# Performance work log

Measured on AMD Instinct MI355X. Metric: run time of the kernel, lower is better.

The kernel has to match this reference:

```python
import jax, jax.numpy as jnp
import numpy as np

SEQ_LEN = 4096
EMBED_DIM = 1280
NUM_HEADS = 16
HEAD_DIM = EMBED_DIM // NUM_HEADS  # 80
SCALING = float(np.sqrt(HEAD_DIM))  # NOTE: source multiplies by sqrt(head_dim)
NEG_INF = float(np.finfo(np.float32).min)


def rotate_half(x):
    x1, x2 = jnp.split(x, 2, axis=-1)
    return jnp.concatenate((-x2, x1), axis=-1)


def setup_inputs() -> dict:
    key = jax.random.key(0)
    ks = jax.random.split(key, 7)
    s = 0.02
    hidden_states = jax.random.normal(ks[0], (SEQ_LEN, EMBED_DIM), dtype=jnp.float32)
    w_qkv = jax.random.normal(ks[1], (3 * EMBED_DIM, EMBED_DIM), dtype=jnp.float32) * s
    b_qkv = jax.random.normal(ks[2], (3 * EMBED_DIM,), dtype=jnp.float32) * s
    w_proj = jax.random.normal(ks[3], (EMBED_DIM, EMBED_DIM), dtype=jnp.float32) * s
    b_proj = jax.random.normal(ks[4], (EMBED_DIM,), dtype=jnp.float32) * s
    # rotary angles: theta duplicated to head_dim (emb = cat(rope, rope))
    inv_freq = 1.0 / (10000.0 ** (jnp.arange(0, HEAD_DIM // 2, dtype=jnp.float32) * 2.0 / HEAD_DIM))
    pos = jnp.arange(SEQ_LEN, dtype=jnp.float32)
    freqs = pos[:, None] * inv_freq[None, :]            # [S, hd/2]
    emb = jnp.concatenate((freqs, freqs), axis=-1)       # [S, hd]
    cos = jnp.cos(emb)
    sin = jnp.sin(emb)
    # 4 packed images of 1024 patches each
    cu_seqlens = jnp.array([0, 1024, 2048, 3072, 4096], dtype=jnp.int32)
    return {
        "hidden_states": hidden_states,
        "w_qkv": w_qkv, "b_qkv": b_qkv,
        "w_proj": w_proj, "b_proj": b_proj,
        "cos": cos, "sin": sin,
        "cu_seqlens": cu_seqlens,
    }


def reference(hidden_states, w_qkv, b_qkv, w_proj, b_proj, cos, sin, cu_seqlens):
    S = hidden_states.shape[0]
    # packed QKV projection
    qkv = hidden_states @ w_qkv.T + b_qkv                  # [S, 3D]
    qkv = qkv.reshape(S, 3, NUM_HEADS, HEAD_DIM)
    q, k, v = qkv[:, 0], qkv[:, 1], qkv[:, 2]              # [S, H, hd]
    # fp32 RoPE (broadcast cos/sin over heads)
    c = cos[:, None, :].astype(jnp.float32)
    sn = sin[:, None, :].astype(jnp.float32)
    qf, kf = q.astype(jnp.float32), k.astype(jnp.float32)
    q = (qf * c + rotate_half(qf) * sn).astype(q.dtype)
    k = (kf * c + rotate_half(kf) * sn).astype(k.dtype)
    # block-diagonal mask from cu_seqlens: same segment -> 0, else -inf
    pos = jnp.arange(S)
    seg = jnp.searchsorted(cu_seqlens, pos, side="right") - 1  # [S]
    bias = jnp.where(seg[:, None] == seg[None, :], 0.0, NEG_INF)  # [S, S]
    # dense attention over whole packed sequence (as in source)
    scores = jnp.einsum("shd,thd->hst", q, k) * SCALING + bias[None]
    weights = jax.nn.softmax(scores.astype(jnp.float32), axis=-1).astype(q.dtype)
    attn = jnp.einsum("hst,thd->shd", weights, v).reshape(S, EMBED_DIM)
    return attn @ w_proj.T + b_proj
```

## Files before the change

kernel.cpp:

```cpp
#include <hip/hip_runtime.h>

#define SEQ   4096
#define EMB   1280
#define NH    16
#define HD    80
#define HDP   96
#define O3    3840
#define SEGLEN 1024
#define NSEG  4
#define QSCALE (8.94427190999915878564f * 1.44269504088896340736f)

typedef unsigned short u16;
typedef __attribute__((ext_vector_type(8))) _Float16 f16x8;
typedef __attribute__((ext_vector_type(4))) _Float16 f16x4;
typedef __attribute__((ext_vector_type(2))) __fp16   h16x2;
typedef __attribute__((ext_vector_type(4))) float    f32x4;

__device__ __forceinline__ float ex2(float x) { return __builtin_amdgcn_exp2f(x); }

__device__ __forceinline__ u16 f2h(float f) {
  union { _Float16 h; u16 u; } v; v.h = (_Float16)f; return v.u;
}
__device__ __forceinline__ float h2f(u16 b) {
  union { u16 u; _Float16 h; } v; v.u = b; return (float)v.h;
}
__device__ __forceinline__ f32x4 exp2_4(f32x4 x) {
  f32x4 r; r.x = ex2(x.x); r.y = ex2(x.y); r.z = ex2(x.z); r.w = ex2(x.w); return r;
}
__device__ __forceinline__ f16x4 pk4(f32x4 s) {
  union { h16x2 h[2]; f16x4 f; } u;
  u.h[0] = __builtin_amdgcn_cvt_pkrtz(s.x, s.y);
  u.h[1] = __builtin_amdgcn_cvt_pkrtz(s.z, s.w);
  return u.f;
}
__device__ __forceinline__ void gl2lds16(const u16* g, u16* l) {
  __builtin_amdgcn_global_load_lds(
      (const __attribute__((address_space(1))) unsigned int*)g,
      (__attribute__((address_space(3))) unsigned int*)l, 16, 0, 0);
}

#define CVT_N1 (SEQ * EMB / 4)
#define CVT_N2 (O3 * EMB / 4)
#define CVT_N3 (EMB * EMB / 4)
__global__ void cvt_all_kernel(const float* __restrict__ a, const float* __restrict__ b,
                               const float* __restrict__ c, u16* __restrict__ oa,
                               u16* __restrict__ ob, u16* __restrict__ oc) {
  int i = blockIdx.x * blockDim.x + threadIdx.x;
  const float* src; u16* dst; int j = i;
  if (j < CVT_N1)                { src = a; dst = oa; }
  else if (j < CVT_N1 + CVT_N2)  { src = b; dst = ob; j -= CVT_N1; }
  else                           { src = c; dst = oc; j -= CVT_N1 + CVT_N2; }
  float4 f = ((const float4*)src)[j];
  union { u16 h[4]; uint2 v; } o;
  o.h[0] = f2h(f.x); o.h[1] = f2h(f.y); o.h[2] = f2h(f.z); o.h[3] = f2h(f.w);
  ((uint2*)dst)[j] = o.v;
}

template<int OUTF>
__global__ __launch_bounds__(256)
void gemm_bias_kernel(const u16* __restrict__ A, const u16* __restrict__ W,
                      const float* __restrict__ bias, void* __restrict__ Cout,
                      int N, int K) {
  __shared__ u16 As[128][64];
  __shared__ u16 Bs[128][64];
  const int tid  = threadIdx.x;
  const int flat = blockIdx.x + gridDim.x * blockIdx.y;
  const int cpx  = (gridDim.x * gridDim.y) >> 3;
  const int nid  = (flat & 7) * cpx + (flat >> 3);
  const int bm   = nid / gridDim.x, bn = nid % gridDim.x;
  const int lane = tid & 63;
  const int wid  = tid >> 6;
  const int wm   = (wid >> 1) * 64, wn = (wid & 1) * 64;
  const int lr   = lane & 15, quad = lane >> 4;

  f32x4 acc[4][4];
  const f32x4 z4 = {0.f, 0.f, 0.f, 0.f};
  #pragma unroll
  for (int i = 0; i < 4; ++i)
    #pragma unroll
    for (int j = 0; j < 4; ++j) acc[i][j] = z4;

  const int arow = tid >> 3;
  const int acol = (((tid & 7) ^ (arow & 7)) * 8);
  const u16* Ab = A + (size_t)(bm * 128) * K;
  const u16* Wb = W + (size_t)(bn * 128) * K;
  u16* AsL = &As[0][0] + tid * 8;
  u16* BsL = &Bs[0][0] + tid * 8;

  for (int kt = 0; kt < K; kt += 64) {
    #pragma unroll
    for (int r = 0; r < 4; ++r) {
      gl2lds16(&Ab[(size_t)(arow + r * 32) * K + kt + acol], AsL + r * 2048);
      gl2lds16(&Wb[(size_t)(arow + r * 32) * K + kt + acol], BsL + r * 2048);
    }
    __syncthreads();
    #pragma unroll
    for (int k32 = 0; k32 < 2; ++k32) {
      const int c = (((k32 * 4 + quad) ^ (lr & 7)) * 8);
      f16x8 aF[4], bF[4];
      #pragma unroll
      for (int i = 0; i < 4; ++i) {
        aF[i] = *(const f16x8*)&As[wm + i * 16 + lr][c];
        bF[i] = *(const f16x8*)&Bs[wn + i * 16 + lr][c];
      }
      #pragma unroll
      for (int i = 0; i < 4; ++i)
        #pragma unroll
        for (int j = 0; j < 4; ++j)
          acc[i][j] = __builtin_amdgcn_mfma_f32_16x16x32_f16(aF[i], bF[j], acc[i][j], 0, 0, 0);
    }
    __syncthreads();
  }

  #pragma unroll
  for (int i = 0; i < 4; ++i) {
    int rowb = bm * 128 + wm + i * 16 + quad * 4;
    #pragma unroll
    for (int j = 0; j < 4; ++j) {
      int col = bn * 128 + wn + j * 16 + lr;
      float bv = bias[col];
      #pragma unroll
      for (int r = 0; r < 4; ++r) {
        float v = acc[i][j][r] + bv;
        if (OUTF) ((float*)Cout)[(size_t)(rowb + r) * N + col] = v;
        else      ((u16*)Cout)[(size_t)(rowb + r) * N + col] = f2h(v);
      }
    }
  }
}

__global__ __launch_bounds__(512, 2)
void gemm256_kernel(const u16* __restrict__ A, const u16* __restrict__ W,
                    const float* __restrict__ bias, u16* __restrict__ Cout,
                    int N, int K) {
  __shared__ u16 As[2][256][64];
  __shared__ u16 Bs[2][256][64];
  const int tid  = threadIdx.x;
  const int flat = blockIdx.x + gridDim.x * blockIdx.y;
  const int cpx  = (gridDim.x * gridDim.y) >> 3;
  const int nid  = (flat & 7) * cpx + (flat >> 3);
  const int bm   = nid / gridDim.x, bn = nid % gridDim.x;
  const int lane = tid & 63;
  const int wid  = tid >> 6;
  const int wm   = wid >> 2;
  const int wn   = wid & 3;
  const int lr   = lane & 15, quad = lane >> 4;
  const int NT   = K >> 6;

  const u16* Ab = A + (size_t)(bm * 256) * K;
  const u16* Wb = W + (size_t)(bn * 256) * K;

  const int srr  = tid >> 3;
  const int scol = ((tid & 7) ^ (srr & 7)) << 3;
  const u16* ApL = Ab + (size_t)srr * K + scol;
  const u16* WpL = Wb + (size_t)srr * K + scol;

  auto stA = [&](int b, int row0, int t) {
    gl2lds16(ApL + (size_t)row0 * K + t * 64,        &As[b][row0][0]      + tid * 8);
    gl2lds16(ApL + (size_t)(row0 + 64) * K + t * 64, &As[b][row0 + 64][0] + tid * 8);
  };
  auto stB = [&](int b, int row0, int t) {
    gl2lds16(WpL + (size_t)row0 * K + t * 64,        &Bs[b][row0][0]      + tid * 8);
    gl2lds16(WpL + (size_t)(row0 + 64) * K + t * 64, &Bs[b][row0 + 64][0] + tid * 8);
  };

  f32x4 acc[8][4];
  const f32x4 z4 = {0.f, 0.f, 0.f, 0.f};
  #pragma unroll
  for (int i = 0; i < 8; ++i)
    #pragma unroll
    for (int j = 0; j < 4; ++j) acc[i][j] = z4;

  const int c0 = (((0 * 4 + quad) ^ (lr & 7)) << 3);
  const int c1 = (((1 * 4 + quad) ^ (lr & 7)) << 3);

  stA(0, 0, 0); stA(0, 128, 0);
  stB(0, 0, 0); stB(0, 128, 0);
  stA(1, 0, 1);
  asm volatile("s_waitcnt vmcnt(2)" ::: "memory");
  __builtin_amdgcn_s_barrier();
  __builtin_amdgcn_sched_barrier(0);

  for (int t = 0; t < NT; ++t) {
    const int buf = t & 1, nb = buf ^ 1;

    f16x8 bF[2][4], aF0[2][4];
    #pragma unroll
    for (int j = 0; j < 4; ++j) {
      bF[0][j] = *(const f16x8*)&Bs[buf][wn * 64 + j * 16 + lr][c0];
      bF[1][j] = *(const f16x8*)&Bs[buf][wn * 64 + j * 16 + lr][c1];
    }
    #pragma unroll
    for (int i = 0; i < 4; ++i) {
      aF0[0][i] = *(const f16x8*)&As[buf][wm * 64 + i * 16 + lr][c0];
      aF0[1][i] = *(const f16x8*)&As[buf][wm * 64 + i * 16 + lr][c1];
    }
    __builtin_amdgcn_sched_barrier(0);
    if (t + 1 < NT) { stB(nb, 0, t + 1); stB(nb, 128, t + 1); stA(nb, 128, t + 1); }
    __builtin_amdgcn_sched_barrier(0);
    __builtin_amdgcn_s_setprio(1);
    #pragma unroll
    for (int k32 = 0; k32 < 2; ++k32)
      #pragma unroll
      for (int i = 0; i < 4; ++i)
        #pragma unroll
        for (int j = 0; j < 4; ++j)
          acc[i][j] = __builtin_amdgcn_mfma_f32_16x16x32_f16(aF0[k32][i], bF[k32][j], acc[i][j], 0, 0, 0);
    __builtin_amdgcn_s_setprio(0);
    __builtin_amdgcn_sched_barrier(0);
    __builtin_amdgcn_s_barrier();

    f16x8 aF1[2][4];
    #pragma unroll
    for (int i = 0; i < 4; ++i) {
      aF1[0][i] = *(const f16x8*)&As[buf][128 + wm * 64 + i * 16 + lr][c0];
      aF1[1][i] = *(const f16x8*)&As[buf][128 + wm * 64 + i * 16 + lr][c1];
    }
    __builtin_amdgcn_sched_barrier(0);
    if (t + 2 < NT) stA(buf, 0, t + 2);
    __builtin_amdgcn_sched_barrier(0);
    __builtin_amdgcn_s_setprio(1);
    #pragma unroll
    for (int k32 = 0; k32 < 2; ++k32)
      #pragma unroll
      for (int i = 0; i < 4; ++i)
        #pragma unroll
        for (int j = 0; j < 4; ++j)
          acc[4 + i][j] = __builtin_amdgcn_mfma_f32_16x16x32_f16(aF1[k32][i], bF[k32][j], acc[4 + i][j], 0, 0, 0);
    __builtin_amdgcn_s_setprio(0);
    if (t < NT - 2) asm volatile("s_waitcnt vmcnt(2)" ::: "memory");
    else            asm volatile("s_waitcnt vmcnt(0)" ::: "memory");
    __builtin_amdgcn_s_barrier();
    __builtin_amdgcn_sched_barrier(0);
  }

  #pragma unroll
  for (int mq = 0; mq < 2; ++mq) {
    #pragma unroll
    for (int i = 0; i < 4; ++i) {
      const int rowb = bm * 256 + mq * 128 + wm * 64 + i * 16 + quad * 4;
      #pragma unroll
      for (int j = 0; j < 4; ++j) {
        const int col = bn * 256 + wn * 64 + j * 16 + lr;
        const float bv = bias[col];
        #pragma unroll
        for (int r = 0; r < 4; ++r)
          Cout[(size_t)(rowb + r) * N + col] = f2h(acc[mq * 4 + i][j][r] + bv);
      }
    }
  }
}

__global__ __launch_bounds__(256)
void rope_reorg_kernel(const u16* __restrict__ qkv, const float* __restrict__ cosp,
                       const float* __restrict__ sinp, u16* __restrict__ Qp,
                       u16* __restrict__ Kp, u16* __restrict__ Vt) {
  __shared__ u16 Qs[64][80];
  __shared__ u16 Ks[64][80];
  __shared__ u16 Vs[64][88];
  const int tid = threadIdx.x;
  const int s0 = blockIdx.x * 64;
  const int h  = blockIdx.y;

  for (int t = tid; t < 640; t += 256) {
    int r = t / 10, c = (t % 10) * 8;
    size_t g = (size_t)(s0 + r) * O3 + h * HD + c;
    *(uint4*)&Qs[r][c] = *(const uint4*)&qkv[g];
    *(uint4*)&Ks[r][c] = *(const uint4*)&qkv[g + EMB];
    *(uint4*)&Vs[r][c] = *(const uint4*)&qkv[g + 2 * EMB];
  }
  __syncthreads();

  for (int t = tid; t < 64 * 24; t += 256) {
    int r = t / 24, d4 = (t % 24) * 4;
    int s = s0 + r;
    size_t po = ((size_t)h * SEQ + s) * HDP + d4;
    if (d4 >= HD) {
      uint2 z = make_uint2(0, 0);
      *(uint2*)&Qp[po] = z; *(uint2*)&Kp[po] = z;
      continue;
    }
    float4 cv = *(const float4*)&cosp[(size_t)s * HD + d4];
    float4 sv = *(const float4*)&sinp[(size_t)s * HD + d4];
    int dp4 = (d4 < 40) ? d4 + 40 : d4 - 40;
    float sgn = (d4 < 40) ? -1.f : 1.f;
    union { u16 h[4]; uint2 v; } oq, ok;
    const float* cp = (const float*)&cv;
    const float* sp = (const float*)&sv;
    #pragma unroll
    for (int j = 0; j < 4; ++j) {
      float q  = h2f(Qs[r][d4 + j]),  k  = h2f(Ks[r][d4 + j]);
      float qp = h2f(Qs[r][dp4 + j]), kp = h2f(Ks[r][dp4 + j]);
      oq.h[j] = f2h((q * cp[j] + sgn * qp * sp[j]) * QSCALE);
      ok.h[j] = f2h(k * cp[j] + sgn * kp * sp[j]);
    }
    *(uint2*)&Qp[po] = oq.v;
    *(uint2*)&Kp[po] = ok.v;
  }

  for (int t = tid; t < HD * 8; t += 256) {
    int d = t / 8, sc = (t % 8) * 8;
    union { u16 h[8]; uint4 v; } o;
    #pragma unroll
    for (int j = 0; j < 8; ++j) o.h[j] = Vs[sc + j][d];
    *(uint4*)&Vt[((size_t)(h * HD + d)) * SEQ + s0 + sc] = o.v;
  }
}

__global__ __launch_bounds__(512)
void attn_kernel(const u16* __restrict__ Qp, const u16* __restrict__ Kp,
                 const u16* __restrict__ Vt, u16* __restrict__ attnO) {
  __shared__ u16 K_l[3][64][96];
  __shared__ u16 V_l[3][96][64];
  const int BUFSZ = 6144;

  const int tid = threadIdx.x;
  const int lane = tid & 63, w = tid >> 6;
  const int lr = lane & 15, quad = lane >> 4;
  const int flat = blockIdx.x + 8 * blockIdx.y + 128 * blockIdx.z;
  const int nid  = (flat & 7) * 64 + (flat >> 3);
  const int qb   = nid & 7;
  const int h    = (nid >> 3) & 15;
  const int sg   = nid >> 7;
  const int seg0 = sg * SEGLEN;
  const int q0b = seg0 + qb * 128;

  f16x8 qF[3];
  {
    int qrow = q0b + w * 16 + lr;
    #pragma unroll
    for (int kc = 0; kc < 3; ++kc)
      qF[kc] = *(const f16x8*)&Qp[((size_t)h * SEQ + qrow) * HDP + kc * 32 + quad * 8];
  }
  asm volatile("" :: "v"(qF[0]), "v"(qF[1]), "v"(qF[2]));
  asm volatile("s_waitcnt vmcnt(0)" ::: "memory");

  {
    u16 val = (tid < 32) ? (u16)0x3C00 : (u16)0;
    #pragma unroll
    for (int b = 0; b < 3; ++b) {
      u16* q = &V_l[0][0][0] + b * BUFSZ + 80 * 64 + tid * 2;
      q[0] = val; q[1] = val;
    }
  }

  const u16* Kbase = Kp + ((size_t)h * SEQ + seg0) * HDP;
  const u16* Vbase = Vt + (size_t)h * HD * SEQ + seg0;
  const u16* pG[3]; u16* dB[3]; int gAdv[3];
  #pragma unroll
  for (int t = 0; t < 3; ++t) {
    int s = t * 512 + tid;
    if (s < 768) {
      int r = s / 12, c = s % 12;
      int ck = (c & ~3) | ((c & 3) ^ ((r >> 1) & 3));
      pG[t] = Kbase + (size_t)r * HDP + ck * 8;
      dB[t] = &K_l[0][0][0] + s * 8;
      gAdv[t] = 64 * HDP;
    } else {
      int sv = (s < 1408) ? s - 768 : s - 1408;
      int rv = sv / 8, cv = sv % 8;
      int cg = cv ^ (rv & 7);
      pG[t] = Vbase + (size_t)rv * SEQ + cg * 8;
      dB[t] = &V_l[0][0][0] + sv * 8;
      gAdv[t] = 64;
    }
  }

  auto stage_adv = [&](int b) {
    #pragma unroll
    for (int t = 0; t < 3; ++t) {
      gl2lds16(pG[t], dB[t] + b * BUFSZ);
      pG[t] += gAdv[t];
    }
  };

  const f32x4 z4 = {0.f, 0.f, 0.f, 0.f};
  float m_r = -3.0e38f;
  f32x4 Oacc[6];
  #pragma unroll
  for (int n = 0; n < 6; ++n) Oacc[n] = z4;

  const int kswz = (lr >> 1) & 3;

  stage_adv(0);
  stage_adv(1);
  asm volatile("s_waitcnt vmcnt(3) lgkmcnt(0)" ::: "memory");
  __builtin_amdgcn_s_barrier();
  __builtin_amdgcn_sched_barrier(0);

  int buf = 0, sb = 2;
  for (int kt = 0; kt < SEGLEN; kt += 64) {
    if (kt + 128 < SEGLEN) stage_adv(sb);

    const u16* kb = &K_l[0][0][0] + buf * BUFSZ;
    const u16* vb = &V_l[0][0][0] + buf * BUFSZ;

    f32x4 S[4];
    __builtin_amdgcn_s_setprio(1);
    #pragma unroll
    for (int ct = 0; ct < 4; ++ct) {
      S[ct] = z4;
      #pragma unroll
      for (int kc = 0; kc < 3; ++kc) {
        f16x8 kF = *(const f16x8*)&kb[(ct * 16 + lr) * 96 + kc * 32 + ((quad ^ kswz) << 3)];
        S[ct] = __builtin_amdgcn_mfma_f32_16x16x32_f16(kF, qF[kc], S[ct], 0, 0, 0);
      }
    }
    __builtin_amdgcn_s_setprio(0);

    float mx = fmaxf(fmaxf(S[0].x, S[0].y), fmaxf(S[0].z, S[0].w));
    #pragma unroll
    for (int ct = 1; ct < 4; ++ct)
      mx = fmaxf(mx, fmaxf(fmaxf(S[ct].x, S[ct].y), fmaxf(S[ct].z, S[ct].w)));
    mx = fmaxf(mx, __shfl_xor(mx, 16, 64));
    mx = fmaxf(mx, __shfl_xor(mx, 32, 64));
    float mnew = fmaxf(m_r, mx);
    float alpha = ex2(m_r - mnew);
    m_r = mnew;

    f32x4 mv = {mnew, mnew, mnew, mnew};
    #pragma unroll
    for (int ct = 0; ct < 4; ++ct) S[ct] = exp2_4(S[ct] - mv);

    if (__ballot(alpha != 1.0f)) {
      f32x4 al;
      al.x = __shfl(alpha, quad * 4 + 0, 64);
      al.y = __shfl(alpha, quad * 4 + 1, 64);
      al.z = __shfl(alpha, quad * 4 + 2, 64);
      al.w = __shfl(alpha, quad * 4 + 3, 64);
      #pragma unroll
      for (int n = 0; n < 6; ++n) Oacc[n] *= al;
    }

    f16x4 pF[4];
    #pragma unroll
    for (int ct = 0; ct < 4; ++ct) pF[ct] = pk4(S[ct]);

    __builtin_amdgcn_s_setprio(1);
    #pragma unroll
    for (int ct = 0; ct < 4; ++ct) {
      const int cchunk = 2 * ct + (quad >> 1);
      #pragma unroll
      for (int n = 0; n < 6; ++n) {
        int vrow = n * 16 + lr;
        const u16* vp = vb + vrow * 64 + ((cchunk ^ (vrow & 7)) << 3) + ((quad & 1) << 2);
        f16x4 vF = *(const f16x4*)vp;
        Oacc[n] = __builtin_amdgcn_mfma_f32_16x16x16f16(pF[ct], vF, Oacc[n], 0, 0, 0);
      }
    }
    __builtin_amdgcn_s_setprio(0);

    if (kt + 128 < SEGLEN) asm volatile("s_waitcnt vmcnt(3)" ::: "memory");
    else                   asm volatile("s_waitcnt vmcnt(0)" ::: "memory");
    __builtin_amdgcn_s_barrier();
    __builtin_amdgcn_sched_barrier(0);

    buf = (buf == 2) ? 0 : buf + 1;
    sb  = (sb == 2) ? 0 : sb + 1;
  }

  f32x4 linv;
  linv.x = 1.0f / __shfl(Oacc[5].x, quad << 4, 64);
  linv.y = 1.0f / __shfl(Oacc[5].y, quad << 4, 64);
  linv.z = 1.0f / __shfl(Oacc[5].z, quad << 4, 64);
  linv.w = 1.0f / __shfl(Oacc[5].w, quad << 4, 64);
  #pragma unroll
  for (int n = 0; n < 5; ++n) {
    int rowb = q0b + w * 16 + quad * 4;
    int col = h * HD + n * 16 + lr;
    attnO[(size_t)(rowb + 0) * EMB + col] = f2h(Oacc[n].x * linv.x);
    attnO[(size_t)(rowb + 1) * EMB + col] = f2h(Oacc[n].y * linv.y);
    attnO[(size_t)(rowb + 2) * EMB + col] = f2h(Oacc[n].z * linv.z);
    attnO[(size_t)(rowb + 3) * EMB + col] = f2h(Oacc[n].w * linv.w);
  }
}

extern "C" void kernel_launch(void* const* d_in, const int* in_sizes, int n_in,
                              void* d_out, int out_size, void* d_ws, size_t ws_size,
                              hipStream_t stream) {
  const float* hs     = (const float*)d_in[0];
  const float* w_qkv  = (const float*)d_in[1];
  const float* b_qkv  = (const float*)d_in[2];
  const float* w_proj = (const float*)d_in[3];
  const float* b_proj = (const float*)d_in[4];
  const float* cosp   = (const float*)d_in[5];
  const float* sinp   = (const float*)d_in[6];
  float* out = (float*)d_out;

  char* p = (char*)d_ws;
  auto take = [&](size_t bytes) { char* q = p; p += (bytes + 255) & ~(size_t)255; return q; };
  u16* hsH    = (u16*)take((size_t)SEQ * EMB * 2);
  u16* wqkvH  = (u16*)take((size_t)O3 * EMB * 2);
  u16* wprojH = (u16*)take((size_t)EMB * EMB * 2);
  u16* qkvO   = (u16*)take((size_t)SEQ * O3 * 2);
  u16* Qp     = (u16*)take((size_t)NH * SEQ * HDP * 2);
  u16* Kp     = (u16*)take((size_t)NH * SEQ * HDP * 2);
  u16* Vt     = (u16*)take((size_t)NH * HD * SEQ * 2);
  u16* attnH  = (u16*)take((size_t)SEQ * EMB * 2);

  int ncvt = (CVT_N1 + CVT_N2 + CVT_N3) / 256;
  cvt_all_kernel<<<ncvt, 256, 0, stream>>>(hs, w_qkv, w_proj, hsH, wqkvH, wprojH);

  gemm256_kernel<<<dim3(O3 / 256, SEQ / 256), 512, 0, stream>>>(hsH, wqkvH, b_qkv, qkvO, O3, EMB);

  rope_reorg_kernel<<<dim3(SEQ / 64, NH), 256, 0, stream>>>(qkvO, cosp, sinp, Qp, Kp, Vt);

  attn_kernel<<<dim3(SEGLEN / 128, NH, NSEG), 512, 0, stream>>>(Qp, Kp, Vt, attnH);

  gemm_bias_kernel<1><<<dim3(EMB / 128, SEQ / 128), 256, 0, stream>>>(attnH, wprojH, b_proj, out, EMB, EMB);
}
```

Measured before the change: 225.3 us.

## Software-pipeline QK^T of next tile with softmax and PV of current tile

```diff
diff --git a/kernel.cpp b/kernel.cpp
--- a/kernel.cpp
+++ b/kernel.cpp
@@ -313,6 +313,7 @@
   __shared__ u16 K_l[3][64][96];
   __shared__ u16 V_l[3][96][64];
   const int BUFSZ = 6144;
+  const int NT = SEGLEN / 64;
 
   const int tid = threadIdx.x;
   const int lane = tid & 63, w = tid >> 6;
@@ -382,20 +383,7 @@
 
   const int kswz = (lr >> 1) & 3;
 
-  stage_adv(0);
-  stage_adv(1);
-  asm volatile("s_waitcnt vmcnt(3) lgkmcnt(0)" ::: "memory");
-  __builtin_amdgcn_s_barrier();
-  __builtin_amdgcn_sched_barrier(0);
-
-  int buf = 0, sb = 2;
-  for (int kt = 0; kt < SEGLEN; kt += 64) {
-    if (kt + 128 < SEGLEN) stage_adv(sb);
-
-    const u16* kb = &K_l[0][0][0] + buf * BUFSZ;
-    const u16* vb = &V_l[0][0][0] + buf * BUFSZ;
-
-    f32x4 S[4];
+  auto qk = [&](f32x4 (&S)[4], const u16* kb) {
     __builtin_amdgcn_s_setprio(1);
     #pragma unroll
     for (int ct = 0; ct < 4; ++ct) {
@@ -407,7 +395,9 @@
       }
     }
     __builtin_amdgcn_s_setprio(0);
-
+  };
+
+  auto smpv = [&](f32x4 (&S)[4], const u16* vb) {
     float mx = fmaxf(fmaxf(S[0].x, S[0].y), fmaxf(S[0].z, S[0].w));
     #pragma unroll
     for (int ct = 1; ct < 4; ++ct)
@@ -449,14 +439,37 @@
       }
     }
     __builtin_amdgcn_s_setprio(0);
-
-    if (kt + 128 < SEGLEN) asm volatile("s_waitcnt vmcnt(3)" ::: "memory");
-    else                   asm volatile("s_waitcnt vmcnt(0)" ::: "memory");
+  };
+
+  stage_adv(0);
+  stage_adv(1);
+  asm volatile("s_waitcnt vmcnt(3) lgkmcnt(0)" ::: "memory");
+  __builtin_amdgcn_s_barrier();
+  __builtin_amdgcn_sched_barrier(0);
+
+  f32x4 Sa[4], Sb[4];
+  qk(Sa, &K_l[0][0][0]);
+
+  int buf = 0, sb = 2;
+  auto iter = [&](int t, f32x4 (&Scur)[4], f32x4 (&Snext)[4]) {
+    if (t + 2 < NT) {
+      stage_adv(sb);
+      asm volatile("s_waitcnt vmcnt(3)" ::: "memory");
+    } else {
+      asm volatile("s_waitcnt vmcnt(0)" ::: "memory");
+    }
     __builtin_amdgcn_s_barrier();
-    __builtin_amdgcn_sched_barrier(0);
-
-    buf = (buf == 2) ? 0 : buf + 1;
-    sb  = (sb == 2) ? 0 : sb + 1;
+    const int nbuf = (buf == 2) ? 0 : buf + 1;
+    if (t + 1 < NT) qk(Snext, &K_l[0][0][0] + nbuf * BUFSZ);
+    smpv(Scur, &V_l[0][0][0] + buf * BUFSZ);
+    __builtin_amdgcn_sched_barrier(0);
+    __builtin_amdgcn_s_barrier();
+    buf = nbuf;
+    sb = (sb == 2) ? 0 : sb + 1;
+  };
+  for (int tt = 0; tt < NT; tt += 2) {
+    iter(tt, Sa, Sb);
+    iter(tt + 1, Sb, Sa);
   }
 
   f32x4 linv;
```

Result: slower. 230.2 us (+2.1%).
